# Performance work log

Measured on AMD Instinct MI355X. Metric: run time of the kernel, lower is better.

The kernel has to match this reference:

```python
import jax, jax.numpy as jnp
import numpy as np

N = 30000      # paper nodes
E = 300000     # edges per etype
IN = 128       # in_feats
HID = 128      # n_hidden
H, D = 4, 32   # n_heads, head dim (HID // H)
C = 16         # n_classes
T = 2          # n_etypes
SLOPE = 0.2    # GATConv leaky-relu negative slope


def setup_inputs() -> dict:
    key = jax.random.key(0)
    ks = jax.random.split(key, 24)
    def w(k, shape, fan):
        return jax.random.normal(k, shape, jnp.float32) * (fan ** -0.5)
    inp = {}
    inp["x"] = jax.random.normal(ks[0], (N, IN), jnp.float32)
    inp["src0"] = jax.random.randint(ks[1], (E,), 0, N, jnp.int32)
    inp["dst0"] = jax.random.randint(ks[2], (E,), 0, N, jnp.int32)
    inp["src1"] = jax.random.randint(ks[3], (E,), 0, N, jnp.int32)
    inp["dst1"] = jax.random.randint(ks[4], (E,), 0, N, jnp.int32)
    # layer 1: in_feats -> H*D, per etype (stacked on leading etype axis)
    inp["W1"]  = w(ks[5], (T, IN, H * D), IN)
    inp["al1"] = w(ks[6], (T, H, D), D)
    inp["ar1"] = w(ks[7], (T, H, D), D)
    inp["b1"]  = jnp.zeros((T, H * D), jnp.float32)
    # layers 2,3: HID -> H*D
    inp["W2"]  = w(ks[8], (T, HID, H * D), HID)
    inp["al2"] = w(ks[9], (T, H, D), D)
    inp["ar2"] = w(ks[10], (T, H, D), D)
    inp["b2"]  = jnp.zeros((T, H * D), jnp.float32)
    inp["W3"]  = w(ks[11], (T, HID, H * D), HID)
    inp["al3"] = w(ks[12], (T, H, D), D)
    inp["ar3"] = w(ks[13], (T, H, D), D)
    inp["b3"]  = jnp.zeros((T, H * D), jnp.float32)
    # output linear
    inp["Wout"] = w(ks[14], (HID, C), HID)
    inp["bout"] = jnp.zeros((C,), jnp.float32)
    return inp


def _gat(h, src, dst, W, al, ar, b):
    """Single-etype GATConv. h:[N,F], W:[F,H*D], al/ar:[H,D], b:[H*D] -> [N,H,D]."""
    feat = (h @ W).reshape(N, H, D)                       # [N,H,D]
    el = jnp.sum(feat * al, axis=-1)                      # [N,H]
    er = jnp.sum(feat * ar, axis=-1)                      # [N,H]
    e = jax.nn.leaky_relu(el[src] + er[dst], SLOPE)       # [E,H]
    # edge softmax over incoming edges of each dst node, per head
    m = jax.ops.segment_max(e, dst, num_segments=N)       # [N,H]
    ex = jnp.exp(e - m[dst])                              # [E,H]
    s = jax.ops.segment_sum(ex, dst, num_segments=N)      # [N,H]
    alpha = ex / s[dst]                                   # [E,H]
    msg = feat[src] * alpha[:, :, None]                   # [E,H,D]
    out = jax.ops.segment_sum(msg, dst, num_segments=N)   # [N,H,D]
    return out + b.reshape(1, H, D)


def _hetero_layer(h, srcs, dsts, W, al, ar, b):
    # HeteroGraphConv: sum-aggregate GATConv outputs across etypes, then flatten heads
    out = _gat(h, srcs[0], dsts[0], W[0], al[0], ar[0], b[0])
    for t in range(1, T):
        out = out + _gat(h, srcs[t], dsts[t], W[t], al[t], ar[t], b[t])
    return out.reshape(N, H * D)


def reference(x, src0, dst0, src1, dst1,
              W1, al1, ar1, b1, W2, al2, ar2, b2, W3, al3, ar3, b3,
              Wout, bout):
    srcs, dsts = (src0, src1), (dst0, dst1)
    h = _hetero_layer(x, srcs, dsts, W1, al1, ar1, b1)
    h = jax.nn.relu(h)  # dropout omitted (eval mode)
    h = _hetero_layer(h, srcs, dsts, W2, al2, ar2, b2)
    h = jax.nn.relu(h)
    h = _hetero_layer(h, srcs, dsts, W3, al3, ar3, b3)
    return h @ Wout + bout  # [N, C]
```

## Files before the change

### kernel.cpp

```cpp
#include <hip/hip_runtime.h>

#define NN 30000
#define EE 300000
#define HH 4
#define SLOPE 0.2f
#define SCAN_NB 15

typedef _Float16 f16;
struct f16x2 { f16 x, y; };
typedef f16 f16x8 __attribute__((ext_vector_type(8)));
typedef float f32x4 __attribute__((ext_vector_type(4)));

__global__ __launch_bounds__(256) void zero_k(int4* __restrict__ p, int n4) {
    const int i = blockIdx.x * 256 + threadIdx.x;
    if (i < n4) p[i] = make_int4(0, 0, 0, 0);
}

__global__ __launch_bounds__(256) void xconv_k(const float* __restrict__ x,
                                               f16* __restrict__ xh) {
    const int i = blockIdx.x * 256 + threadIdx.x;
    const float4 a = reinterpret_cast<const float4*>(x)[i * 2];
    const float4 b = reinterpret_cast<const float4*>(x)[i * 2 + 1];
    union { f16 h[8]; float4 f4; } pk;
    pk.h[0] = (f16)a.x; pk.h[1] = (f16)a.y; pk.h[2] = (f16)a.z; pk.h[3] = (f16)a.w;
    pk.h[4] = (f16)b.x; pk.h[5] = (f16)b.y; pk.h[6] = (f16)b.z; pk.h[7] = (f16)b.w;
    reinterpret_cast<float4*>(xh)[i] = pk.f4;
}

__global__ __launch_bounds__(256) void wconv3_k(const float* __restrict__ W0,
                                                const float* __restrict__ W1,
                                                const float* __restrict__ W2,
                                                f16* __restrict__ Wh) {
    const int l = blockIdx.z, t = blockIdx.y;
    const float* W = (l == 0) ? W0 : ((l == 1) ? W1 : W2);
    f16* Whl = Wh + (size_t)l * 2 * 16384;
    const int i0 = blockIdx.x * 2048;
    #pragma unroll
    for (int j = 0; j < 8; ++j) {
        const int i = i0 + threadIdx.x + j * 256;
        const int k = i >> 7, col = i & 127;
        Whl[t * 16384 + col * 128 + k] = (f16)W[t * 16384 + i];
    }
}

#define APAD 136
__global__ __launch_bounds__(256) void gemm_mfma(const f16* __restrict__ Ah,
                                                 const f16* __restrict__ Whbase,
                                                 const float* __restrict__ albase,
                                                 const float* __restrict__ arbase,
                                                 f16* __restrict__ featbase,
                                                 float* __restrict__ elbase,
                                                 float* __restrict__ erbase) {
    __shared__ f16 Asl[64 * APAD];
    __shared__ f16 Bsl[128 * APAD];
    const int et = blockIdx.y;
    const f16* Wh = Whbase + et * 16384;
    f16* feat = featbase + (size_t)et * NN * 128;
    const int row0 = blockIdx.x * 64;
    const int t = threadIdx.x;

    #pragma unroll
    for (int j = 0; j < 4; ++j) {
        const int idx = t + j * 256;
        const int r = idx >> 4, q = idx & 15;
        const int row = row0 + r;
        float4 v = make_float4(0.f, 0.f, 0.f, 0.f);
        if (row < NN) v = reinterpret_cast<const float4*>(Ah + (size_t)row * 128)[q];
        *reinterpret_cast<float4*>(&Asl[r * APAD + q * 8]) = v;
    }
    #pragma unroll
    for (int j = 0; j < 8; ++j) {
        const int idx = t + j * 256;
        const int col = idx >> 4, k16 = idx & 15;
        *reinterpret_cast<float4*>(&Bsl[col * APAD + k16 * 8]) =
            *reinterpret_cast<const float4*>(Wh + col * 128 + k16 * 8);
    }
    __syncthreads();

    const int w = t >> 6, lane = t & 63;
    const int r = lane & 15, g = lane >> 4;
    const int mb = w * 16;
    f32x4 acc[8];
    #pragma unroll
    for (int nt = 0; nt < 8; ++nt) acc[nt] = (f32x4){0.f, 0.f, 0.f, 0.f};

    #pragma unroll
    for (int ks = 0; ks < 4; ++ks) {
        const f16x8 av = *reinterpret_cast<const f16x8*>(&Asl[(mb + r) * APAD + ks * 32 + g * 8]);
        #pragma unroll
        for (int nt = 0; nt < 8; ++nt) {
            const f16x8 bv =
                *reinterpret_cast<const f16x8*>(&Bsl[(nt * 16 + r) * APAD + ks * 32 + g * 8]);
            acc[nt] = __builtin_amdgcn_mfma_f32_16x16x32_f16(av, bv, acc[nt], 0, 0, 0);
        }
    }

    float alv[8], arv[8];
    #pragma unroll
    for (int nt = 0; nt < 8; ++nt) {
        alv[nt] = albase[et * 128 + nt * 16 + r];
        arv[nt] = arbase[et * 128 + nt * 16 + r];
    }
    #pragma unroll
    for (int p = 0; p < 4; ++p) {
        const int row = row0 + mb + g * 4 + p;
        const bool ok = row < NN;
        if (ok) {
            #pragma unroll
            for (int nt = 0; nt < 8; ++nt)
                feat[(size_t)row * 128 + nt * 16 + r] = (f16)acc[nt][p];
        }
        #pragma unroll
        for (int h = 0; h < 4; ++h) {
            float pl = fmaf(acc[2 * h][p], alv[2 * h], acc[2 * h + 1][p] * alv[2 * h + 1]);
            float pr = fmaf(acc[2 * h][p], arv[2 * h], acc[2 * h + 1][p] * arv[2 * h + 1]);
            pl += __shfl_xor(pl, 1); pl += __shfl_xor(pl, 2);
            pl += __shfl_xor(pl, 4); pl += __shfl_xor(pl, 8);
            pr += __shfl_xor(pr, 1); pr += __shfl_xor(pr, 2);
            pr += __shfl_xor(pr, 4); pr += __shfl_xor(pr, 8);
            if (ok && r == 0) {
                elbase[et * NN * HH + row * HH + h] = pl;
                erbase[et * NN * HH + row * HH + h] = pr;
            }
        }
    }
}

__global__ __launch_bounds__(256) void hist_k(const int* __restrict__ dst0,
                                              const int* __restrict__ dst1,
                                              int* __restrict__ deg) {
    const int e = blockIdx.x * 256 + threadIdx.x;
    if (e >= EE) return;
    const int t = blockIdx.y;
    const int* d = t ? dst1 : dst0;
    atomicAdd(&deg[t * NN + d[e]], 1);
}

__global__ __launch_bounds__(256) void scan1_k(const int* __restrict__ deg,
                                               int* __restrict__ offs,
                                               int* __restrict__ blocksum) {
    const int t = blockIdx.y, b = blockIdx.x;
    const int* d = deg + t * NN;
    int* o = offs + t * (NN + 1);
    const int base = b * 2048 + threadIdx.x * 8;
    int v[8];
    int s = 0;
    #pragma unroll
    for (int j = 0; j < 8; ++j) {
        const int i = base + j;
        v[j] = (i < NN) ? d[i] : 0;
        s += v[j];
    }
    __shared__ int buf[256];
    buf[threadIdx.x] = s;
    __syncthreads();
    #pragma unroll
    for (int ofs = 1; ofs < 256; ofs <<= 1) {
        const int add = (threadIdx.x >= (unsigned)ofs) ? buf[threadIdx.x - ofs] : 0;
        __syncthreads();
        buf[threadIdx.x] += add;
        __syncthreads();
    }
    int run = buf[threadIdx.x] - s;
    #pragma unroll
    for (int j = 0; j < 8; ++j) {
        const int i = base + j;
        if (i < NN) o[i] = run;
        run += v[j];
    }
    if (threadIdx.x == 255) blocksum[t * SCAN_NB + b] = buf[255];
}

__global__ __launch_bounds__(64) void scan2_k(int* __restrict__ blocksum,
                                              int* __restrict__ offs) {
    if (threadIdx.x != 0) return;
    #pragma unroll
    for (int t = 0; t < 2; ++t) {
        int run = 0;
        for (int b = 0; b < SCAN_NB; ++b) {
            const int v = blocksum[t * SCAN_NB + b];
            blocksum[t * SCAN_NB + b] = run;
            run += v;
        }
        offs[t * (NN + 1) + NN] = run;
    }
}

__global__ __launch_bounds__(256) void scan3_k(int* __restrict__ offs,
                                               const int* __restrict__ blocksum,
                                               int* __restrict__ cursor) {
    const int t = blockIdx.y, b = blockIdx.x;
    const int boff = blocksum[t * SCAN_NB + b];
    int* o = offs + t * (NN + 1);
    int* cur = cursor + t * NN;
    const int base = b * 2048 + threadIdx.x * 8;
    #pragma unroll
    for (int j = 0; j < 8; ++j) {
        const int i = base + j;
        if (i < NN) {
            const int val = o[i] + boff;
            o[i] = val;
            cur[i] = val;
        }
    }
}

__global__ __launch_bounds__(256) void scatter_k(const int* __restrict__ src0,
                                                 const int* __restrict__ dst0,
                                                 const int* __restrict__ src1,
                                                 const int* __restrict__ dst1,
                                                 int* __restrict__ cursor,
                                                 int* __restrict__ csr_src) {
    const int e = blockIdx.x * 256 + threadIdx.x;
    if (e >= EE) return;
    const int t = blockIdx.y;
    const int* s = t ? src1 : src0;
    const int* d = t ? dst1 : dst0;
    const int pos = atomicAdd(&cursor[t * NN + d[e]], 1);
    csr_src[t * EE + pos] = s[e];
}

__global__ __launch_bounds__(256) void pull_agg2_k(const int* __restrict__ csr_src,
                                                   const int* __restrict__ offs,
                                                   const float* __restrict__ el,
                                                   const float* __restrict__ er,
                                                   const f16* __restrict__ feat,
                                                   const float* __restrict__ b0,
                                                   const float* __restrict__ b1,
                                                   f16* __restrict__ out, int relu) {
    __shared__ float xb[2][2][128];
    const int w = threadIdx.x >> 6, lane = threadIdx.x & 63;
    const int p = w >> 1, t = w & 1;
    const int n = blockIdx.x * 2 + p;
    const int c0 = lane * 2;
    const int h = c0 >> 5;

    const int* so = offs + t * (NN + 1);
    const int e0 = so[n], e1 = so[n + 1];
    const float erh = er[t * NN * HH + n * HH + h];
    const int* cs = csr_src + t * EE;
    const f16* ft = feat + (size_t)t * NN * 128;
    const float* elt = el + t * NN * HH;
    float sA = 0.f, x0A = 0.f, x1A = 0.f;
    float sB = 0.f, x0B = 0.f, x1B = 0.f;
    float sC = 0.f, x0C = 0.f, x1C = 0.f;
    float sD = 0.f, x0D = 0.f, x1D = 0.f;
    int e = e0;
    for (; e + 3 < e1; e += 4) {
        const int sa = cs[e], sb = cs[e + 1], sc = cs[e + 2], sd = cs[e + 3];
        float va = elt[sa * HH + h] + erh;
        float vb = elt[sb * HH + h] + erh;
        float vc = elt[sc * HH + h] + erh;
        float vd = elt[sd * HH + h] + erh;
        const f16x2 fa = *reinterpret_cast<const f16x2*>(ft + (size_t)sa * 128 + c0);
        const f16x2 fb = *reinterpret_cast<const f16x2*>(ft + (size_t)sb * 128 + c0);
        const f16x2 fc = *reinterpret_cast<const f16x2*>(ft + (size_t)sc * 128 + c0);
        const f16x2 fd = *reinterpret_cast<const f16x2*>(ft + (size_t)sd * 128 + c0);
        va = (va >= 0.f) ? va : va * SLOPE;
        vb = (vb >= 0.f) ? vb : vb * SLOPE;
        vc = (vc >= 0.f) ? vc : vc * SLOPE;
        vd = (vd >= 0.f) ? vd : vd * SLOPE;
        const float ea = __expf(va), eb = __expf(vb);
        const float ec = __expf(vc), ed = __expf(vd);
        sA += ea; x0A = fmaf(ea, (float)fa.x, x0A); x1A = fmaf(ea, (float)fa.y, x1A);
        sB += eb; x0B = fmaf(eb, (float)fb.x, x0B); x1B = fmaf(eb, (float)fb.y, x1B);
        sC += ec; x0C = fmaf(ec, (float)fc.x, x0C); x1C = fmaf(ec, (float)fc.y, x1C);
        sD += ed; x0D = fmaf(ed, (float)fd.x, x0D); x1D = fmaf(ed, (float)fd.y, x1D);
    }
    for (; e < e1; ++e) {
        const int sa = cs[e];
        float va = elt[sa * HH + h] + erh;
        va = (va >= 0.f) ? va : va * SLOPE;
        const float ea = __expf(va);
        const f16x2 fa = *reinterpret_cast<const f16x2*>(ft + (size_t)sa * 128 + c0);
        sA += ea; x0A = fmaf(ea, (float)fa.x, x0A); x1A = fmaf(ea, (float)fa.y, x1A);
    }
    const float s = (sA + sB) + (sC + sD);
    const float inv = (s > 0.f) ? 1.f / s : 0.f;
    xb[p][t][c0]     = ((x0A + x0B) + (x0C + x0D)) * inv;
    xb[p][t][c0 + 1] = ((x1A + x1B) + (x1C + x1D)) * inv;
    __syncthreads();
    if (t == 0) {
        float a0 = xb[p][0][c0] + xb[p][1][c0] + b0[c0] + b1[c0];
        float a1 = xb[p][0][c0 + 1] + xb[p][1][c0 + 1] + b0[c0 + 1] + b1[c0 + 1];
        if (relu) { a0 = fmaxf(a0, 0.f); a1 = fmaxf(a1, 0.f); }
        f16x2 o; o.x = (f16)a0; o.y = (f16)a1;
        *reinterpret_cast<f16x2*>(out + (size_t)n * 128 + c0) = o;
    }
}

__global__ __launch_bounds__(256) void out_gemm_k(const f16* __restrict__ A,
                                                  const float* __restrict__ W,
                                                  const float* __restrict__ bout,
                                                  float* __restrict__ out) {
    __shared__ float At[16][132];
    const int row0 = blockIdx.x * 16;
    const int t = threadIdx.x;
    {
        const int r = t >> 4, c8 = t & 15;
        const f16x8 v = *reinterpret_cast<const f16x8*>(A + (size_t)(row0 + r) * 128 + c8 * 8);
        #pragma unroll
        for (int j = 0; j < 8; ++j) At[r][c8 * 8 + j] = (float)v[j];
    }
    __syncthreads();
    const int r = t >> 4, c = t & 15;
    float accv = 0.f;
    #pragma unroll 8
    for (int k = 0; k < 128; ++k) accv = fmaf(At[r][k], W[k * 16 + c], accv);
    out[(row0 + r) * 16 + c] = accv + bout[c];
}

extern "C" void kernel_launch(void* const* d_in, const int* in_sizes, int n_in,
                              void* d_out, int out_size, void* d_ws, size_t ws_size,
                              hipStream_t stream) {
    (void)in_sizes; (void)n_in; (void)out_size; (void)ws_size;
    const float* x = (const float*)d_in[0];
    const int* src0 = (const int*)d_in[1];
    const int* dst0 = (const int*)d_in[2];
    const int* src1 = (const int*)d_in[3];
    const int* dst1 = (const int*)d_in[4];
    const float* W[3]  = {(const float*)d_in[5], (const float*)d_in[9],  (const float*)d_in[13]};
    const float* al[3] = {(const float*)d_in[6], (const float*)d_in[10], (const float*)d_in[14]};
    const float* ar[3] = {(const float*)d_in[7], (const float*)d_in[11], (const float*)d_in[15]};
    const float* bb[3] = {(const float*)d_in[8], (const float*)d_in[12], (const float*)d_in[16]};
    const float* Wout = (const float*)d_in[17];
    const float* bout = (const float*)d_in[18];
    float* outp = (float*)d_out;

    char* pb = (char*)d_ws;
    f16* feat   = (f16*)pb;    pb += (size_t)2 * NN * 128 * 2;
    f16* xh     = (f16*)pb;    pb += (size_t)NN * 128 * 2;
    f16* hbuf   = (f16*)pb;    pb += (size_t)NN * 128 * 2;
    float* el   = (float*)pb;  pb += (size_t)2 * NN * HH * 4;
    float* er   = (float*)pb;  pb += (size_t)2 * NN * HH * 4;
    int* deg    = (int*)pb;    pb += (size_t)2 * NN * 4;
    int* cursor = (int*)pb;    pb += (size_t)2 * NN * 4;
    int* offs   = (int*)pb;    pb += (size_t)2 * (NN + 1) * 4;
    int* bsum   = (int*)pb;    pb += (size_t)2 * SCAN_NB * 4;
    f16* Wh     = (f16*)pb;    pb += (size_t)3 * 2 * 128 * 128 * 2;
    int* csr    = (int*)pb;    pb += (size_t)2 * EE * 4;

    zero_k<<<(2 * NN / 4 + 255) / 256, 256, 0, stream>>>((int4*)deg, 2 * NN / 4);
    hist_k<<<dim3((EE + 255) / 256, 2), 256, 0, stream>>>(dst0, dst1, deg);
    scan1_k<<<dim3(SCAN_NB, 2), 256, 0, stream>>>(deg, offs, bsum);
    scan2_k<<<1, 64, 0, stream>>>(bsum, offs);
    scan3_k<<<dim3(SCAN_NB, 2), 256, 0, stream>>>(offs, bsum, cursor);
    scatter_k<<<dim3((EE + 255) / 256, 2), 256, 0, stream>>>(src0, dst0, src1, dst1, cursor, csr);
    wconv3_k<<<dim3(8, 2, 3), 256, 0, stream>>>(W[0], W[1], W[2], Wh);
    xconv_k<<<NN * 128 / 8 / 256, 256, 0, stream>>>(x, xh);

    const f16* hin = xh;
    for (int l = 0; l < 3; ++l) {
        gemm_mfma<<<dim3((NN + 63) / 64, 2), 256, 0, stream>>>(hin, Wh + l * 2 * 16384,
                                                               al[l], ar[l], feat, el, er);
        pull_agg2_k<<<NN / 2, 256, 0, stream>>>(csr, offs, el, er, feat,
                                                bb[l], bb[l] + 128, hbuf, (l < 2) ? 1 : 0);
        hin = hbuf;
    }
    out_gemm_k<<<NN / 16, 256, 0, stream>>>(hbuf, Wout, bout, outp);
}
```

Before: 266.3 us.

## Precompute per-edge attention exponentials in a separate edge kernel

Adds a per-edge kernel that computes leaky-relu and exp of el[src]+er[dst] for all four heads at once and stores them in CSR order, and records destination indices during the scatter. The pull aggregation then reads these precomputed values instead of gathering el and recomputing exp in each lane. In the old kernel, the 16 lanes covering one head each recomputed the same exp for every edge. The change removes that redundancy but adds a kernel launch per layer, an extra edge-sized csr_dst array, and a 9.6 MB exponential buffer written and read back per layer.

```diff
diff --git a/kernel.cpp b/kernel.cpp
--- a/kernel.cpp
+++ b/kernel.cpp
@@ -210,20 +210,43 @@
                                                  const int* __restrict__ src1,
                                                  const int* __restrict__ dst1,
                                                  int* __restrict__ cursor,
-                                                 int* __restrict__ csr_src) {
+                                                 int* __restrict__ csr_src,
+                                                 int* __restrict__ csr_dst) {
     const int e = blockIdx.x * 256 + threadIdx.x;
     if (e >= EE) return;
     const int t = blockIdx.y;
     const int* s = t ? src1 : src0;
     const int* d = t ? dst1 : dst0;
-    const int pos = atomicAdd(&cursor[t * NN + d[e]], 1);
+    const int di = d[e];
+    const int pos = atomicAdd(&cursor[t * NN + di], 1);
     csr_src[t * EE + pos] = s[e];
-}
-
-__global__ __launch_bounds__(256) void pull_agg2_k(const int* __restrict__ csr_src,
+    csr_dst[t * EE + pos] = di;
+}
+
+__global__ __launch_bounds__(256) void edge_ex_k(const int* __restrict__ csr_src,
+                                                 const int* __restrict__ csr_dst,
+                                                 const float* __restrict__ el,
+                                                 const float* __restrict__ er,
+                                                 float* __restrict__ exf) {
+    const int i = blockIdx.x * 256 + threadIdx.x;
+    if (i >= EE) return;
+    const int t = blockIdx.y;
+    const int s = csr_src[t * EE + i];
+    const int d = csr_dst[t * EE + i];
+    const float4 l4 = *reinterpret_cast<const float4*>(el + t * NN * HH + s * 4);
+    const float4 r4 = *reinterpret_cast<const float4*>(er + t * NN * HH + d * 4);
+    float4 o;
+    float v;
+    v = l4.x + r4.x; v = (v >= 0.f) ? v : v * SLOPE; o.x = __expf(v);
+    v = l4.y + r4.y; v = (v >= 0.f) ? v : v * SLOPE; o.y = __expf(v);
+    v = l4.z + r4.z; v = (v >= 0.f) ? v : v * SLOPE; o.z = __expf(v);
+    v = l4.w + r4.w; v = (v >= 0.f) ? v : v * SLOPE; o.w = __expf(v);
+    *reinterpret_cast<float4*>(exf + (size_t)t * EE * 4 + (size_t)i * 4) = o;
+}
+
+__global__ __launch_bounds__(256) void pull_agg3_k(const int* __restrict__ csr_src,
                                                    const int* __restrict__ offs,
-                                                   const float* __restrict__ el,
-                                                   const float* __restrict__ er,
+                                                   const float* __restrict__ exf,
                                                    const f16* __restrict__ feat,
                                                    const float* __restrict__ b0,
                                                    const float* __restrict__ b1,
@@ -237,10 +260,9 @@
 
     const int* so = offs + t * (NN + 1);
     const int e0 = so[n], e1 = so[n + 1];
-    const float erh = er[t * NN * HH + n * HH + h];
     const int* cs = csr_src + t * EE;
+    const float* ext = exf + (size_t)t * EE * 4;
     const f16* ft = feat + (size_t)t * NN * 128;
-    const float* elt = el + t * NN * HH;
     float sA = 0.f, x0A = 0.f, x1A = 0.f;
     float sB = 0.f, x0B = 0.f, x1B = 0.f;
     float sC = 0.f, x0C = 0.f, x1C = 0.f;
@@ -248,20 +270,14 @@
     int e = e0;
     for (; e + 3 < e1; e += 4) {
         const int sa = cs[e], sb = cs[e + 1], sc = cs[e + 2], sd = cs[e + 3];
-        float va = elt[sa * HH + h] + erh;
-        float vb = elt[sb * HH + h] + erh;
-        float vc = elt[sc * HH + h] + erh;
-        float vd = elt[sd * HH + h] + erh;
+        const float ea = ext[(size_t)e * 4 + h];
+        const float eb = ext[(size_t)(e + 1) * 4 + h];
+        const float ec = ext[(size_t)(e + 2) * 4 + h];
+        const float ed = ext[(size_t)(e + 3) * 4 + h];
         const f16x2 fa = *reinterpret_cast<const f16x2*>(ft + (size_t)sa * 128 + c0);
         const f16x2 fb = *reinterpret_cast<const f16x2*>(ft + (size_t)sb * 128 + c0);
         const f16x2 fc = *reinterpret_cast<const f16x2*>(ft + (size_t)sc * 128 + c0);
         const f16x2 fd = *reinterpret_cast<const f16x2*>(ft + (size_t)sd * 128 + c0);
-        va = (va >= 0.f) ? va : va * SLOPE;
-        vb = (vb >= 0.f) ? vb : vb * SLOPE;
-        vc = (vc >= 0.f) ? vc : vc * SLOPE;
-        vd = (vd >= 0.f) ? vd : vd * SLOPE;
-        const float ea = __expf(va), eb = __expf(vb);
-        const float ec = __expf(vc), ed = __expf(vd);
         sA += ea; x0A = fmaf(ea, (float)fa.x, x0A); x1A = fmaf(ea, (float)fa.y, x1A);
         sB += eb; x0B = fmaf(eb, (float)fb.x, x0B); x1B = fmaf(eb, (float)fb.y, x1B);
         sC += ec; x0C = fmaf(ec, (float)fc.x, x0C); x1C = fmaf(ec, (float)fc.y, x1C);
@@ -269,9 +285,7 @@
     }
     for (; e < e1; ++e) {
         const int sa = cs[e];
-        float va = elt[sa * HH + h] + erh;
-        va = (va >= 0.f) ? va : va * SLOPE;
-        const float ea = __expf(va);
+        const float ea = ext[(size_t)e * 4 + h];
         const f16x2 fa = *reinterpret_cast<const f16x2*>(ft + (size_t)sa * 128 + c0);
         sA += ea; x0A = fmaf(ea, (float)fa.x, x0A); x1A = fmaf(ea, (float)fa.y, x1A);
     }
@@ -339,13 +353,16 @@
     int* bsum   = (int*)pb;    pb += (size_t)2 * SCAN_NB * 4;
     f16* Wh     = (f16*)pb;    pb += (size_t)3 * 2 * 128 * 128 * 2;
     int* csr    = (int*)pb;    pb += (size_t)2 * EE * 4;
+    int* csrd   = (int*)pb;    pb += (size_t)2 * EE * 4;
+    float* exf  = (float*)pb;  pb += (size_t)2 * EE * HH * 4;
 
     zero_k<<<(2 * NN / 4 + 255) / 256, 256, 0, stream>>>((int4*)deg, 2 * NN / 4);
     hist_k<<<dim3((EE + 255) / 256, 2), 256, 0, stream>>>(dst0, dst1, deg);
     scan1_k<<<dim3(SCAN_NB, 2), 256, 0, stream>>>(deg, offs, bsum);
     scan2_k<<<1, 64, 0, stream>>>(bsum, offs);
     scan3_k<<<dim3(SCAN_NB, 2), 256, 0, stream>>>(offs, bsum, cursor);
-    scatter_k<<<dim3((EE + 255) / 256, 2), 256, 0, stream>>>(src0, dst0, src1, dst1, cursor, csr);
+    scatter_k<<<dim3((EE + 255) / 256, 2), 256, 0, stream>>>(src0, dst0, src1, dst1,
+                                                             cursor, csr, csrd);
     wconv3_k<<<dim3(8, 2, 3), 256, 0, stream>>>(W[0], W[1], W[2], Wh);
     xconv_k<<<NN * 128 / 8 / 256, 256, 0, stream>>>(x, xh);
 
@@ -353,7 +370,8 @@
     for (int l = 0; l < 3; ++l) {
         gemm_mfma<<<dim3((NN + 63) / 64, 2), 256, 0, stream>>>(hin, Wh + l * 2 * 16384,
                                                                al[l], ar[l], feat, el, er);
-        pull_agg2_k<<<NN / 2, 256, 0, stream>>>(csr, offs, el, er, feat,
+        edge_ex_k<<<dim3((EE + 255) / 256, 2), 256, 0, stream>>>(csr, csrd, el, er, exf);
+        pull_agg3_k<<<NN / 2, 256, 0, stream>>>(csr, offs, exf, feat,
                                                 bb[l], bb[l] + 128, hbuf, (l < 2) ? 1 : 0);
         hin = hbuf;
     }
```

New measurement: 282.7 us. 6.2% more time.
